# Kernel optimization log

Measured on AMD Instinct MI355X. Metric: run time of the kernel, lower is better.

The kernel has to match this reference:

```python
import jax, jax.numpy as jnp
import numpy as np

B, S, E, H = 4, 2048, 768, 12
D = E // H  # head_dim = 64


def setup_inputs() -> dict:
    key = jax.random.key(0)
    k1, k2, k3 = jax.random.split(key, 3)
    x = jax.random.normal(k1, (B, S, E), dtype=jnp.float32)
    # torch Linear(E, 3E): weight [3E, E]; we store transposed [E, 3E] for x @ W
    W_qkv = jax.random.normal(k2, (E, 3 * E), dtype=jnp.float32) * (E ** -0.5)
    b_qkv = jax.random.normal(k3, (3 * E,), dtype=jnp.float32) * 0.02
    return {"x": x, "W_qkv": W_qkv, "b_qkv": b_qkv}


def reference(x, W_qkv, b_qkv):
    n, length, embed_dim = x.shape
    qkv = x @ W_qkv + b_qkv                                   # [B, S, 3E]
    qkv = qkv.reshape(n, length, 3, H, D).transpose(2, 0, 3, 1, 4)  # [3, B, H, S, D]
    q, k, v = qkv[0], qkv[1], qkv[2]
    scores = jnp.einsum('bhsd,bhtd->bhst', q, k) * (D ** -0.5)  # [B, H, S, S]
    attn = jax.nn.softmax(scores, axis=-1)
    out = jnp.einsum('bhst,bhtd->bhsd', attn, v)               # [B, H, S, D]
    return out.transpose(0, 2, 1, 3).reshape(n, length, embed_dim)
```

## Files before the change

kernel.cpp:

```cpp
#include <hip/hip_runtime.h>
#include <cmath>

#define B_ 4
#define S_ 2048
#define E_ 768
#define H_ 12
#define D_ 64
#define NE3 (3*E_)
#define QKV_ELEMS ((size_t)B_*H_*S_*D_)

typedef __attribute__((ext_vector_type(8)))  short bf16x8;
typedef __attribute__((ext_vector_type(4)))  float f32x4;
typedef __attribute__((ext_vector_type(16))) float f32x16;

__device__ __forceinline__ unsigned short f2bf(float f) {
    union { float f; unsigned u; } v; v.f = f;
    return (unsigned short)((v.u + 0x7FFFu + ((v.u >> 16) & 1u)) >> 16);
}
__device__ __forceinline__ float exp2_fast(float x) {
    float r; asm("v_exp_f32 %0, %1" : "=v"(r) : "v"(x)); return r;
}
__device__ __forceinline__ float max3f(float a, float b, float c) {
    float r; asm("v_max3_f32 %0, %1, %2, %3" : "=v"(r) : "v"(a), "v"(b), "v"(c));
    return r;
}
#define LOG2E 1.44269504088896340736f

__global__ __launch_bounds__(256)
void cvt_x(const float* __restrict__ x, unsigned short* __restrict__ xb)
{
    const size_t i = ((size_t)blockIdx.x * 256 + threadIdx.x) * 8;
    float4 a = *(const float4*)(x + i);
    float4 b = *(const float4*)(x + i + 4);
    ushort4 o0, o1;
    o0.x = f2bf(a.x); o0.y = f2bf(a.y); o0.z = f2bf(a.z); o0.w = f2bf(a.w);
    o1.x = f2bf(b.x); o1.y = f2bf(b.y); o1.z = f2bf(b.z); o1.w = f2bf(b.w);
    *(ushort4*)(xb + i)     = o0;
    *(ushort4*)(xb + i + 4) = o1;
}

__global__ __launch_bounds__(256)
void transpose_w(const float* __restrict__ W, unsigned short* __restrict__ Wt)
{
    __shared__ float t[32][33];
    const int tx = threadIdx.x & 31;
    const int ty = threadIdx.x >> 5;
    const int n0 = blockIdx.x * 32;
    const int k0 = blockIdx.y * 32;
    #pragma unroll
    for (int r = 0; r < 4; ++r)
        t[ty + 8*r][tx] = W[(size_t)(k0 + ty + 8*r) * NE3 + n0 + tx];
    __syncthreads();
    #pragma unroll
    for (int r = 0; r < 4; ++r)
        Wt[(size_t)(n0 + ty + 8*r) * E_ + k0 + tx] = f2bf(t[tx][ty + 8*r]);
}

__global__ __launch_bounds__(256, 2)
void qkv_gemm_mfma(const unsigned short* __restrict__ xb,
                   const unsigned short* __restrict__ Wt,
                   const float* __restrict__ bias,
                   unsigned short* __restrict__ qkv,
                   unsigned short* __restrict__ vtg)
{
    __shared__ __align__(16) unsigned short As[128*64];
    __shared__ __align__(16) unsigned short Bs[128*64];

    const int tid  = threadIdx.x;
    const int lane = tid & 63;
    const int wave = tid >> 6;
    const int lo   = lane & 15;
    const int hi   = lane >> 4;
    const int wr   = wave >> 1;
    const int wc   = wave & 1;
    const int nstart = blockIdx.x * 128;
    const int mstart = blockIdx.y * 128;

    f32x4 acc[4][4];
    #pragma unroll
    for (int i = 0; i < 4; ++i)
        #pragma unroll
        for (int j = 0; j < 4; ++j) acc[i][j] = (f32x4){0.f,0.f,0.f,0.f};

    for (int k0 = 0; k0 < E_; k0 += 64) {
        __syncthreads();
        #pragma unroll
        for (int it = 0; it < 4; ++it) {
            const int cid = tid + it*256;
            const int row = cid >> 3, c = cid & 7;
            bf16x8 av = *(const bf16x8*)(xb + (size_t)(mstart + row)*E_ + k0 + c*8);
            *(bf16x8*)&As[row*64 + ((c ^ (row & 7)) * 8)] = av;
            bf16x8 bv = *(const bf16x8*)(Wt + (size_t)(nstart + row)*E_ + k0 + c*8);
            *(bf16x8*)&Bs[row*64 + ((c ^ (row & 7)) * 8)] = bv;
        }
        __syncthreads();

        #pragma unroll
        for (int ks = 0; ks < 2; ++ks) {
            const int c = ks*4 + hi;
            bf16x8 af[4], bfr[4];
            #pragma unroll
            for (int i = 0; i < 4; ++i) {
                const int ar = wr*64 + i*16 + lo;
                af[i] = *(const bf16x8*)&As[ar*64 + ((c ^ (ar & 7)) * 8)];
            }
            #pragma unroll
            for (int j = 0; j < 4; ++j) {
                const int br = wc*64 + j*16 + lo;
                bfr[j] = *(const bf16x8*)&Bs[br*64 + ((c ^ (br & 7)) * 8)];
            }
            #pragma unroll
            for (int i = 0; i < 4; ++i)
                #pragma unroll
                for (int j = 0; j < 4; ++j)
                    acc[i][j] = __builtin_amdgcn_mfma_f32_16x16x32_bf16(
                        af[i], bfr[j], acc[i][j], 0, 0, 0);
        }
    }

    #pragma unroll
    for (int j = 0; j < 4; ++j) {
        const int ncol = nstart + wc*64 + j*16 + lo;
        const int g  = ncol >> 6;
        const int cq = g / H_;
        const int h  = g % H_;
        const int d  = ncol & 63;
        const float bv = bias[ncol];
        const float qscale = (cq == 0) ? 0.125f : 1.0f;
        unsigned short* dst = qkv + (size_t)cq * QKV_ELEMS;
        #pragma unroll
        for (int i = 0; i < 4; ++i) {
            const int mbase = mstart + wr*64 + i*16 + hi*4;
            const int b  = mbase >> 11;
            const int s0 = mbase & 2047;
            if (cq == 2) {
                ushort4 vv;
                vv.x = f2bf(acc[i][j][0] + bv);
                vv.y = f2bf(acc[i][j][1] + bv);
                vv.z = f2bf(acc[i][j][2] + bv);
                vv.w = f2bf(acc[i][j][3] + bv);
                *(ushort4*)(vtg + (((size_t)(b*H_ + h))*D_ + d)*S_ + s0) = vv;
            } else {
                #pragma unroll
                for (int r = 0; r < 4; ++r)
                    dst[(((size_t)(b*H_ + h))*S_ + s0 + r)*D_ + d] =
                        f2bf((acc[i][j][r] + bv) * qscale);
            }
        }
    }
}

__global__ __launch_bounds__(256, 2)
void attn_mfma32(const unsigned short* __restrict__ qkv,
                 const unsigned short* __restrict__ vtg,
                 float* __restrict__ out)
{
    __shared__ __align__(16) unsigned short Ks[2*64*64];
    __shared__ __align__(16) unsigned short Vt[2*64*64];

    const int tid  = threadIdx.x;
    const int lane = tid & 63;
    const int wave = tid >> 6;
    const int q32  = lane & 31;
    const int hi   = lane >> 5;
    const int qtile = blockIdx.x * 128;
    const int bh = blockIdx.y;
    const size_t base  = (size_t)bh * S_ * D_;
    const size_t baseT = (size_t)bh * D_ * S_;

    const unsigned short* Q = qkv;
    const unsigned short* K = qkv + QKV_ELEMS;

    bf16x8 qf[4];
    {
        const size_t qrow = base + (size_t)(qtile + wave*32 + q32) * D_;
        #pragma unroll
        for (int m = 0; m < 4; ++m)
            qf[m] = *(const bf16x8*)(Q + qrow + m*16 + hi*8);
    }

    const int kkey0 = tid >> 3,          kch0 = tid & 7;
    const int kkey1 = (tid + 256) >> 3,  kch1 = (tid + 256) & 7;
    const int vd0 = tid >> 3, vs0 = tid & 7;
    const int vd1 = vd0 + 32;

    #define GLOADK(kc_, buf_) do {                                                   \
        __builtin_amdgcn_global_load_lds(                                            \
            (const __attribute__((address_space(1))) unsigned*)                      \
                (K + base + (size_t)((kc_) + kkey0)*D_ + ((kch0 ^ (kkey0 & 7))*8)),  \
            (__attribute__((address_space(3))) unsigned*)&Ks[(buf_)*4096 + tid*8],   \
            16, 0, 0);                                                               \
        __builtin_amdgcn_global_load_lds(                                            \
            (const __attribute__((address_space(1))) unsigned*)                      \
                (K + base + (size_t)((kc_) + kkey1)*D_ + ((kch1 ^ (kkey1 & 7))*8)),  \
            (__attribute__((address_space(3))) unsigned*)&Ks[(buf_)*4096 + (tid+256)*8], \
            16, 0, 0);                                                               \
    } while (0)
    #define GLOADV(kc_, buf_) do {                                                   \
        __builtin_amdgcn_global_load_lds(                                            \
            (const __attribute__((address_space(1))) unsigned*)                      \
                (vtg + baseT + (size_t)vd0*S_ + (kc_) + ((vs0 ^ (vd0 & 7))*8)),      \
            (__attribute__((address_space(3))) unsigned*)&Vt[(buf_)*4096 + tid*8],   \
            16, 0, 0);                                                               \
        __builtin_amdgcn_global_load_lds(                                            \
            (const __attribute__((address_space(1))) unsigned*)                      \
                (vtg + baseT + (size_t)vd1*S_ + (kc_) + ((vs0 ^ (vd1 & 7))*8)),      \
            (__attribute__((address_space(3))) unsigned*)&Vt[(buf_)*4096 + (tid+256)*8], \
            16, 0, 0);                                                               \
    } while (0)

    f32x16 o0, o1;
    #pragma unroll
    for (int r = 0; r < 16; ++r) { o0[r] = 0.f; o1[r] = 0.f; }
    float m_run = -INFINITY, l_run = 0.f;

    GLOADK(0, 0);
    GLOADV(0, 0);
    __syncthreads();
    int cur = 0;

    for (int kc = 0; kc < S_; kc += 64) {
        const int nkc = (kc + 64 < S_) ? (kc + 64) : 0;
        GLOADK(nkc, cur ^ 1);
        GLOADV(nkc, cur ^ 1);

        const int o = cur * 4096;

        f32x16 sg[2];
        __builtin_amdgcn_s_setprio(1);
        #pragma unroll
        for (int g = 0; g < 2; ++g) {
            f32x16 acc;
            #pragma unroll
            for (int r = 0; r < 16; ++r) acc[r] = 0.f;
            const int key = g*32 + q32;
            #pragma unroll
            for (int m = 0; m < 4; ++m) {
                const int c = m*2 + hi;
                bf16x8 kf = *(const bf16x8*)&Ks[o + key*64 + ((c ^ (key & 7)) * 8)];
                acc = __builtin_amdgcn_mfma_f32_32x32x16_bf16(kf, qf[m], acc, 0, 0, 0);
            }
            sg[g] = acc;
        }
        __builtin_amdgcn_s_setprio(0);

        float m0 = fmaxf(sg[0][0], sg[0][1]);
        float m1 = fmaxf(sg[0][8], sg[0][9]);
        float m2 = fmaxf(sg[1][0], sg[1][1]);
        float m3 = fmaxf(sg[1][8], sg[1][9]);
        #pragma unroll
        for (int r = 2; r < 8; r += 2) {
            m0 = max3f(m0, sg[0][r],   sg[0][r+1]);
            m1 = max3f(m1, sg[0][r+8], sg[0][r+9]);
            m2 = max3f(m2, sg[1][r],   sg[1][r+1]);
            m3 = max3f(m3, sg[1][r+8], sg[1][r+9]);
        }
        float mx = fmaxf(fmaxf(m0, m1), fmaxf(m2, m3));
        mx = fmaxf(mx, __shfl_xor(mx, 32));

        if (__any(mx > m_run + 8.0f)) {
            const float mn    = fmaxf(m_run, mx);
            const float alpha = exp2_fast((m_run - mn) * LOG2E);
            m_run = mn;
            l_run *= alpha;
            #pragma unroll
            for (int r = 0; r < 16; ++r) { o0[r] *= alpha; o1[r] *= alpha; }
        }
        const float nmnL = -m_run * LOG2E;

        #pragma unroll
        for (int r = 0; r < 16; ++r) sg[0][r] = exp2_fast(fmaf(sg[0][r], LOG2E, nmnL));
        #pragma unroll
        for (int r = 0; r < 16; ++r) sg[1][r] = exp2_fast(fmaf(sg[1][r], LOG2E, nmnL));

        float a8[8];
        #pragma unroll
        for (int r = 0; r < 8; ++r) a8[r] = (sg[0][r] + sg[0][r+8]) + (sg[1][r] + sg[1][r+8]);
        float a4_0 = a8[0] + a8[4], a4_1 = a8[1] + a8[5];
        float a4_2 = a8[2] + a8[6], a4_3 = a8[3] + a8[7];
        float psum = (a4_0 + a4_1) + (a4_2 + a4_3);
        psum += __shfl_xor(psum, 32);
        l_run += psum;

        unsigned U0[8], U1[8];
        #pragma unroll
        for (int c2 = 0; c2 < 8; ++c2) {
            asm("v_cvt_pk_bf16_f32 %0, %1, %2"
                : "=v"(U0[c2]) : "v"(sg[0][2*c2]), "v"(sg[0][2*c2+1]));
            asm("v_cvt_pk_bf16_f32 %0, %1, %2"
                : "=v"(U1[c2]) : "v"(sg[1][2*c2]), "v"(sg[1][2*c2+1]));
        }

        unsigned R0[2][2], R1[2][2];
        #pragma unroll
        for (int tb = 0; tb < 2; ++tb)
            #pragma unroll
            for (int w2 = 0; w2 < 2; ++w2) {
                unsigned s0 = hi ? U0[4*tb + w2] : U0[4*tb + 2 + w2];
                unsigned s1 = hi ? U1[4*tb + w2] : U1[4*tb + 2 + w2];
                R0[tb][w2] = (unsigned)__shfl_xor((int)s0, 32);
                R1[tb][w2] = (unsigned)__shfl_xor((int)s1, 32);
            }

        __builtin_amdgcn_s_setprio(1);
        #pragma unroll
        for (int t = 0; t < 4; ++t) {
            const int tb = t & 1;
            union { unsigned w[4]; bf16x8 v; } pw;
            if (t < 2) {
                pw.w[0] = hi ? R0[tb][0] : U0[4*tb + 0];
                pw.w[1] = hi ? R0[tb][1] : U0[4*tb + 1];
                pw.w[2] = hi ? U0[4*tb + 2] : R0[tb][0];
                pw.w[3] = hi ? U0[4*tb + 3] : R0[tb][1];
            } else {
                pw.w[0] = hi ? R1[tb][0] : U1[4*tb + 0];
                pw.w[1] = hi ? R1[tb][1] : U1[4*tb + 1];
                pw.w[2] = hi ? U1[4*tb + 2] : R1[tb][0];
                pw.w[3] = hi ? U1[4*tb + 3] : R1[tb][1];
            }
            const int c = t*2 + hi;
            {
                const int d = q32;
                bf16x8 vf = *(const bf16x8*)&Vt[o + d*64 + ((c ^ (d & 7)) * 8)];
                o0 = __builtin_amdgcn_mfma_f32_32x32x16_bf16(vf, pw.v, o0, 0, 0, 0);
            }
            {
                const int d = 32 + q32;
                bf16x8 vf = *(const bf16x8*)&Vt[o + d*64 + ((c ^ (d & 7)) * 8)];
                o1 = __builtin_amdgcn_mfma_f32_32x32x16_bf16(vf, pw.v, o1, 0, 0, 0);
            }
        }
        __builtin_amdgcn_s_setprio(0);

        __syncthreads();
        cur ^= 1;
    }

    const int b = bh / H_;
    const int h = bh % H_;
    const float inv = 1.f / l_run;
    const int qglob = qtile + wave*32 + q32;
    float* obase = out + ((size_t)b*S_ + qglob)*E_ + h*64;
    #pragma unroll
    for (int rg = 0; rg < 4; ++rg) {
        float4 w0 = { o0[4*rg+0]*inv, o0[4*rg+1]*inv, o0[4*rg+2]*inv, o0[4*rg+3]*inv };
        *(float4*)(obase + rg*8 + hi*4) = w0;
        float4 w1 = { o1[4*rg+0]*inv, o1[4*rg+1]*inv, o1[4*rg+2]*inv, o1[4*rg+3]*inv };
        *(float4*)(obase + 32 + rg*8 + hi*4) = w1;
    }
    #undef GLOADK
    #undef GLOADV
}

extern "C" void kernel_launch(void* const* d_in, const int* in_sizes, int n_in,
                              void* d_out, int out_size, void* d_ws, size_t ws_size,
                              hipStream_t stream)
{
    (void)in_sizes; (void)n_in; (void)out_size; (void)ws_size;
    const float* x    = (const float*)d_in[0];
    const float* W    = (const float*)d_in[1];
    const float* bias = (const float*)d_in[2];
    float* out = (float*)d_out;

    unsigned short* qkv = (unsigned short*)d_ws;
    unsigned short* xb  = qkv + 3*QKV_ELEMS;
    unsigned short* Wtb = xb + (size_t)B_*S_*E_;
    unsigned short* vtg = Wtb + (size_t)E_*NE3;

    cvt_x<<<(B_*S_*E_)/(256*8), 256, 0, stream>>>(x, xb);
    transpose_w<<<dim3(NE3/32, E_/32), 256, 0, stream>>>(W, Wtb);

    dim3 g1(NE3/128, (B_*S_)/128);
    qkv_gemm_mfma<<<g1, 256, 0, stream>>>(xb, Wtb, bias, qkv, vtg);

    dim3 g2(S_/128, B_*H_);
    attn_mfma32<<<g2, 256, 0, stream>>>(qkv, vtg, out);
}
```

Measured before the change: 138.6 us.

## Split attention over two key halves and merge partials in a combine kernel

Each attention block now handles only half of the key sequence, selected by a new grid z-dimension, which doubles the number of blocks. Each half writes a normalized bf16 partial output plus its running max and sum. A new combine kernel reweights the two partials with the log-sum-exp rule and writes the fp32 output. The intent is better CU occupancy and less tail imbalance on the attention grid. The cost is an extra launch, extra global traffic for the partials, and bf16 rounding of the intermediate outputs.

```diff
diff --git a/kernel.cpp b/kernel.cpp
--- a/kernel.cpp
+++ b/kernel.cpp
@@ -8,6 +8,7 @@
 #define D_ 64
 #define NE3 (3*E_)
 #define QKV_ELEMS ((size_t)B_*H_*S_*D_)
+#define BHS ((size_t)B_*H_*S_)
 
 typedef __attribute__((ext_vector_type(8)))  short bf16x8;
 typedef __attribute__((ext_vector_type(4)))  float f32x4;
@@ -16,6 +17,9 @@
 __device__ __forceinline__ unsigned short f2bf(float f) {
     union { float f; unsigned u; } v; v.f = f;
     return (unsigned short)((v.u + 0x7FFFu + ((v.u >> 16) & 1u)) >> 16);
+}
+__device__ __forceinline__ float bf2f(unsigned short u) {
+    union { unsigned u; float f; } v; v.u = (unsigned)u << 16; return v.f;
 }
 __device__ __forceinline__ float exp2_fast(float x) {
     float r; asm("v_exp_f32 %0, %1" : "=v"(r) : "v"(x)); return r;
@@ -153,7 +157,9 @@
 __global__ __launch_bounds__(256, 2)
 void attn_mfma32(const unsigned short* __restrict__ qkv,
                  const unsigned short* __restrict__ vtg,
-                 float* __restrict__ out)
+                 unsigned short* __restrict__ po0,
+                 unsigned short* __restrict__ po1,
+                 float* __restrict__ ml)
 {
     __shared__ __align__(16) unsigned short Ks[2*64*64];
     __shared__ __align__(16) unsigned short Vt[2*64*64];
@@ -165,6 +171,8 @@
     const int hi   = lane >> 5;
     const int qtile = blockIdx.x * 128;
     const int bh = blockIdx.y;
+    const int split = blockIdx.z;
+    const int kbase = split * (S_/2);
     const size_t base  = (size_t)bh * S_ * D_;
     const size_t baseT = (size_t)bh * D_ * S_;
 
@@ -214,13 +222,13 @@
     for (int r = 0; r < 16; ++r) { o0[r] = 0.f; o1[r] = 0.f; }
     float m_run = -INFINITY, l_run = 0.f;
 
-    GLOADK(0, 0);
-    GLOADV(0, 0);
+    GLOADK(kbase, 0);
+    GLOADV(kbase, 0);
     __syncthreads();
     int cur = 0;
 
-    for (int kc = 0; kc < S_; kc += 64) {
-        const int nkc = (kc + 64 < S_) ? (kc + 64) : 0;
+    for (int kc = kbase; kc < kbase + S_/2; kc += 64) {
+        int nkc = kc + 64; if (nkc >= kbase + S_/2) nkc -= S_/2;
         GLOADK(nkc, cur ^ 1);
         GLOADV(nkc, cur ^ 1);
 
@@ -336,20 +344,63 @@
         cur ^= 1;
     }
 
+    const float inv = 1.f / l_run;
+    const int qglob = qtile + wave*32 + q32;
+    unsigned short* prow = (split ? po1 : po0) + ((size_t)bh*S_ + qglob)*64;
+    #pragma unroll
+    for (int rg = 0; rg < 4; ++rg) {
+        ushort4 w0;
+        w0.x = f2bf(o0[4*rg+0]*inv); w0.y = f2bf(o0[4*rg+1]*inv);
+        w0.z = f2bf(o0[4*rg+2]*inv); w0.w = f2bf(o0[4*rg+3]*inv);
+        *(ushort4*)(prow + rg*8 + hi*4) = w0;
+        ushort4 w1;
+        w1.x = f2bf(o1[4*rg+0]*inv); w1.y = f2bf(o1[4*rg+1]*inv);
+        w1.z = f2bf(o1[4*rg+2]*inv); w1.w = f2bf(o1[4*rg+3]*inv);
+        *(ushort4*)(prow + 32 + rg*8 + hi*4) = w1;
+    }
+    if (hi == 0) {
+        float* mlp = ml + ((size_t)split*BHS + (size_t)bh*S_ + qglob)*2;
+        mlp[0] = m_run;
+        mlp[1] = l_run;
+    }
+    #undef GLOADK
+    #undef GLOADV
+}
+
+__global__ __launch_bounds__(256)
+void combine_out(const unsigned short* __restrict__ po0,
+                 const unsigned short* __restrict__ po1,
+                 const float* __restrict__ ml,
+                 float* __restrict__ out)
+{
+    const int tid = threadIdx.x;
+    const int bh  = blockIdx.y;
+    const int s   = blockIdx.x*32 + (tid >> 3);
+    const int d8  = (tid & 7) * 8;
+    const size_t row = (size_t)bh*S_ + s;
+
+    const float mA = ml[row*2],         lA = ml[row*2 + 1];
+    const float mB = ml[(BHS + row)*2], lB = ml[(BHS + row)*2 + 1];
+    const float M  = fmaxf(mA, mB);
+    float wA = lA * exp2_fast((mA - M) * LOG2E);
+    float wB = lB * exp2_fast((mB - M) * LOG2E);
+    const float inv = 1.f / (wA + wB);
+    wA *= inv; wB *= inv;
+
+    ushort4 a0 = *(const ushort4*)(po0 + row*64 + d8);
+    ushort4 a1 = *(const ushort4*)(po0 + row*64 + d8 + 4);
+    ushort4 b0 = *(const ushort4*)(po1 + row*64 + d8);
+    ushort4 b1 = *(const ushort4*)(po1 + row*64 + d8 + 4);
+
     const int b = bh / H_;
     const int h = bh % H_;
-    const float inv = 1.f / l_run;
-    const int qglob = qtile + wave*32 + q32;
-    float* obase = out + ((size_t)b*S_ + qglob)*E_ + h*64;
-    #pragma unroll
-    for (int rg = 0; rg < 4; ++rg) {
-        float4 w0 = { o0[4*rg+0]*inv, o0[4*rg+1]*inv, o0[4*rg+2]*inv, o0[4*rg+3]*inv };
-        *(float4*)(obase + rg*8 + hi*4) = w0;
-        float4 w1 = { o1[4*rg+0]*inv, o1[4*rg+1]*inv, o1[4*rg+2]*inv, o1[4*rg+3]*inv };
-        *(float4*)(obase + 32 + rg*8 + hi*4) = w1;
-    }
-    #undef GLOADK
-    #undef GLOADV
+    float* op = out + ((size_t)b*S_ + s)*E_ + h*64 + d8;
+    float4 r0 = { wA*bf2f(a0.x) + wB*bf2f(b0.x), wA*bf2f(a0.y) + wB*bf2f(b0.y),
+                  wA*bf2f(a0.z) + wB*bf2f(b0.z), wA*bf2f(a0.w) + wB*bf2f(b0.w) };
+    float4 r1 = { wA*bf2f(a1.x) + wB*bf2f(b1.x), wA*bf2f(a1.y) + wB*bf2f(b1.y),
+                  wA*bf2f(a1.z) + wB*bf2f(b1.z), wA*bf2f(a1.w) + wB*bf2f(b1.w) };
+    *(float4*)op       = r0;
+    *(float4*)(op + 4) = r1;
 }
 
 extern "C" void kernel_launch(void* const* d_in, const int* in_sizes, int n_in,
@@ -363,9 +414,12 @@
     float* out = (float*)d_out;
 
     unsigned short* qkv = (unsigned short*)d_ws;
+    unsigned short* po0 = qkv + 2*QKV_ELEMS;
     unsigned short* xb  = qkv + 3*QKV_ELEMS;
+    unsigned short* po1 = xb;
     unsigned short* Wtb = xb + (size_t)B_*S_*E_;
     unsigned short* vtg = Wtb + (size_t)E_*NE3;
+    float*          ml  = (float*)(vtg + QKV_ELEMS);
 
     cvt_x<<<(B_*S_*E_)/(256*8), 256, 0, stream>>>(x, xb);
     transpose_w<<<dim3(NE3/32, E_/32), 256, 0, stream>>>(W, Wtb);
@@ -373,6 +427,9 @@
     dim3 g1(NE3/128, (B_*S_)/128);
     qkv_gemm_mfma<<<g1, 256, 0, stream>>>(xb, Wtb, bias, qkv, vtg);
 
-    dim3 g2(S_/128, B_*H_);
-    attn_mfma32<<<g2, 256, 0, stream>>>(qkv, vtg, out);
-}
+    dim3 g2(S_/128, B_*H_, 2);
+    attn_mfma32<<<g2, 256, 0, stream>>>(qkv, vtg, po0, po1, ml);
+
+    dim3 g3(S_/32, B_*H_);
+    combine_out<<<g3, 256, 0, stream>>>(po0, po1, ml, out);
+}
```

New measurement: 148.2 us. 1.07x slower.
